# Kernel optimization log

Hardware: AMD Instinct MI355X
Metric: run time of the kernel (lower is better)

Reference implementation:

```python
import jax, jax.numpy as jnp
import numpy as np

TAU = 0.02
M = 5  # len(modality_types) + 1; modality 0 == padding


def setup_inputs() -> dict:
    B, Q, S, D = 64, 32, 256, 128
    key = jax.random.key(0)
    k0, k1, k2, k3, k4 = jax.random.split(key, 5)
    q = jax.random.normal(k0, (B, Q, D), dtype=jnp.float32)
    q = q / jnp.linalg.norm(q, axis=-1, keepdims=True)
    d = jax.random.normal(k1, (B, S, D), dtype=jnp.float32)
    d = d / jnp.linalg.norm(d, axis=-1, keepdims=True)
    # guarantee every modality 0..M-1 appears in each doc (first M tokens)
    head = jnp.tile(jnp.arange(M, dtype=jnp.int32), (B, 1))
    rest = jax.random.randint(k2, (B, S - M), 0, M, dtype=jnp.int32)
    modality_ids = jnp.concatenate([head, rest], axis=1)
    query_types = jax.random.randint(k3, (B,), 1, M, dtype=jnp.int32)  # in [1, M-1]
    lengths = jax.random.randint(k4, (B,), Q // 2, Q + 1)
    query_mask = jnp.arange(Q)[None, :] < lengths[:, None]
    return {"query_emb": q, "doc_emb": d, "modality_ids": modality_ids,
            "query_types": query_types, "query_mask": query_mask}


def _loss(query_emb, doc_emb, modality_ids, query_types, query_mask):
    B = query_emb.shape[0]
    idx = jnp.arange(B)
    # token-level similarity: (B, C, Q, S)
    base = jnp.einsum('bqd,csd->bcqs', query_emb, doc_emb)
    qnorm = jnp.maximum(query_mask.sum(axis=1), 1).astype(base.dtype)  # (B,)

    # agg (ColBERT max-sim): max over non-pad doc tokens, masked query sum
    nonpad = (modality_ids != 0)[None, :, None, :]
    agg_max = jnp.where(nonpad, base, -jnp.inf).max(axis=-1)           # (B, C, Q)
    sim = (agg_max * query_mask[:, None, :].astype(base.dtype)).sum(axis=-1)
    sim = sim / qnorm[:, None]                                          # (B, C)

    # _all_modality_sims: segmented max over s per modality, then sum over q
    per_mod = []
    for m in range(M):
        mask_m = (modality_ids == m)[None, :, None, :]
        per_mod.append(jnp.where(mask_m, base, -jnp.inf).max(axis=-1).sum(axis=-1))
    sims = jnp.stack(per_mod, axis=-1)                                  # (B, C, M)
    sims = sims / qnorm[:, None, None]

    # replace diagonal with the query's own modality score
    sim_fixed = sim.at[idx, idx].set(sims[idx, idx, query_types])

    # hard negatives: all (doc, modality) pairs except pad modality and own positive
    all_modal = sims.reshape(B, B * M)
    keep_mask = jnp.ones((B, B * M), dtype=bool)
    keep_mask = keep_mask.at[:, 0::M].set(False)
    keep_mask = keep_mask.at[idx, idx * M + query_types].set(False)
    n_keep = B * M - B - 1  # exact per-row count (query_types >= 1, no overlap)
    order = jnp.argsort((~keep_mask).astype(jnp.int32), axis=1, stable=True)[:, :n_keep]
    extras = jnp.take_along_axis(all_modal, order, axis=1)              # (B, n_keep)

    logits = jnp.concatenate([sim_fixed, extras], axis=1) / TAU
    # cross entropy with labels = arange(B) (positive is column b)
    return (jax.nn.logsumexp(logits, axis=1) - logits[idx, idx]).mean()


def reference(query_emb, doc_emb, modality_ids, query_types, query_mask):
    return _loss(query_emb, doc_emb, modality_ids, query_types, query_mask)
```

## Files before the change

kernel.cpp:

```cpp
#include <hip/hip_runtime.h>
#include <math.h>

#define TAU_F 0.02f
#define NB 64
#define NQ 32
#define NS 256
#define ND 128
#define MAXT 20
#define PERMSTRIDE 320

typedef __bf16 bf16x8 __attribute__((ext_vector_type(8)));
typedef float f32x4 __attribute__((ext_vector_type(4)));

#define OFF_TILEMOD 0u
#define OFF_TCOUNT  5120u
#define OFF_DFRAG   131072u
#define OFF_QFRAG   5373952u
#define OFF_SIMOUT  5898240u

__global__ __launch_bounds__(256) void
prep_frag_kernel(const float* __restrict__ qemb, const float* __restrict__ demb,
                 const int* __restrict__ mod,
                 __bf16* __restrict__ qfrag, __bf16* __restrict__ dfrag,
                 int* __restrict__ tilemod_g, int* __restrict__ tcount_g) {
    int blk = blockIdx.x;
    int tid = threadIdx.x;
    int lane = tid & 63, wv = tid >> 6;
    int quad = lane >> 4, li = lane & 15;

    if (blk >= NB) {
        int b = blk - NB;
#pragma unroll
        for (int i = 0; i < 2; ++i) {
            int combo = wv * 2 + i;
            int qt = combo >> 2, kc = combo & 3;
            int rowq = qt * 16 + li;
            int k0 = kc * 32 + quad * 8;
            const float* src = qemb + ((size_t)b * NQ + rowq) * ND + k0;
            float4 a = *(const float4*)src;
            float4 bq = *(const float4*)(src + 4);
            bf16x8 o;
            o[0] = (__bf16)a.x;  o[1] = (__bf16)a.y;  o[2] = (__bf16)a.z;  o[3] = (__bf16)a.w;
            o[4] = (__bf16)bq.x; o[5] = (__bf16)bq.y; o[6] = (__bf16)bq.z; o[7] = (__bf16)bq.w;
            *(bf16x8*)(qfrag + (((size_t)(b * 2 + qt) * 4 + kc) * 64 + lane) * 8) = o;
        }
        return;
    }

    int c = blk;
    __shared__ int smod[NS];
    __shared__ int sperm[PERMSTRIDE];
    __shared__ int counts[5], firsts[5], offs[5], padded[5];
    __shared__ int stilemod[MAXT];
    __shared__ int sT;

    if (tid < 5) { counts[tid] = 0; firsts[tid] = NS; }
    __syncthreads();
    int m_tok = mod[c * NS + tid];
    smod[tid] = m_tok;
    if (m_tok) { atomicAdd(&counts[m_tok], 1); atomicMin(&firsts[m_tok], tid); }
    __syncthreads();
    if (tid == 0) {
        int pos = 0;
        for (int m = 1; m <= 4; ++m) {
            offs[m] = pos;
            int p = (counts[m] + 15) & ~15;
            padded[m] = p;
            for (int t = pos >> 4; t < (pos + p) >> 4; ++t) stilemod[t] = m;
            pos += p;
        }
        sT = pos >> 4;
        tcount_g[c] = pos >> 4;
    }
    __syncthreads();
    if (m_tok) {
        int rank = 0;
        for (int s = 0; s < tid; ++s) rank += (smod[s] == m_tok);
        sperm[offs[m_tok] + rank] = tid;
    }
    if (tid < 4) {
        int m = tid + 1;
        for (int p = counts[m]; p < padded[m]; ++p) sperm[offs[m] + p] = firsts[m];
    }
    __syncthreads();
    int T = sT;
    if (tid < T) tilemod_g[c * MAXT + tid] = stilemod[tid];

    int kc = wv;
    int k0 = kc * 32 + quad * 8;
    for (int t = 0; t < T; ++t) {
        int srow = sperm[t * 16 + li];
        const float* src = demb + ((size_t)c * NS + srow) * ND + k0;
        float4 a = *(const float4*)src;
        float4 bq = *(const float4*)(src + 4);
        bf16x8 o;
        o[0] = (__bf16)a.x;  o[1] = (__bf16)a.y;  o[2] = (__bf16)a.z;  o[3] = (__bf16)a.w;
        o[4] = (__bf16)bq.x; o[5] = (__bf16)bq.y; o[6] = (__bf16)bq.z; o[7] = (__bf16)bq.w;
        *(bf16x8*)(dfrag + (((size_t)(c * MAXT + t) * 4 + kc) * 64 + lane) * 8) = o;
    }
}

__global__ __launch_bounds__(256) void
main_kernel(const __bf16* __restrict__ dfrag, const __bf16* __restrict__ qfrag,
            const int* __restrict__ tilemod, const int* __restrict__ tcount,
            const int* __restrict__ qmask, float* __restrict__ simout) {
    int blk = blockIdx.x;
    int c = blk >> 5;
    int bp = blk & 31;
    int b0 = bp * 2;
    int tid = threadIdx.x;
    int lane = tid & 63, wv = tid >> 6;

    bf16x8 bfrag[4][4];
#pragma unroll
    for (int qt = 0; qt < 4; ++qt) {
        int bg = b0 + (qt >> 1), qtl = qt & 1;
#pragma unroll
        for (int kc = 0; kc < 4; ++kc)
            bfrag[qt][kc] = *(const bf16x8*)(qfrag + (((size_t)(bg * 2 + qtl) * 4 + kc) * 64 + lane) * 8);
    }

    float vmax[4][4];
#pragma unroll
    for (int m = 0; m < 4; ++m)
#pragma unroll
        for (int qt = 0; qt < 4; ++qt) vmax[m][qt] = -1e30f;

    int T = tcount[c];
    for (int t = wv; t < T; t += 4) {
        bf16x8 af[4];
#pragma unroll
        for (int kc = 0; kc < 4; ++kc)
            af[kc] = *(const bf16x8*)(dfrag + (((size_t)(c * MAXT + t) * 4 + kc) * 64 + lane) * 8);
        float vv[4];
#pragma unroll
        for (int qt = 0; qt < 4; ++qt) {
            f32x4 acc = {0.f, 0.f, 0.f, 0.f};
#pragma unroll
            for (int kc = 0; kc < 4; ++kc)
                acc = __builtin_amdgcn_mfma_f32_16x16x32_bf16(af[kc], bfrag[qt][kc], acc, 0, 0, 0);
            float v = fmaxf(fmaxf(acc[0], acc[1]), fmaxf(acc[2], acc[3]));
            v = fmaxf(v, __shfl_xor(v, 16, 64));
            v = fmaxf(v, __shfl_xor(v, 32, 64));
            vv[qt] = v;
        }
        int tm = tilemod[c * MAXT + t];
        switch (tm) {
        case 1:
#pragma unroll
            for (int qt = 0; qt < 4; ++qt) vmax[0][qt] = fmaxf(vmax[0][qt], vv[qt]);
            break;
        case 2:
#pragma unroll
            for (int qt = 0; qt < 4; ++qt) vmax[1][qt] = fmaxf(vmax[1][qt], vv[qt]);
            break;
        case 3:
#pragma unroll
            for (int qt = 0; qt < 4; ++qt) vmax[2][qt] = fmaxf(vmax[2][qt], vv[qt]);
            break;
        default:
#pragma unroll
            for (int qt = 0; qt < 4; ++qt) vmax[3][qt] = fmaxf(vmax[3][qt], vv[qt]);
            break;
        }
    }

    __shared__ float lv[4][4][4][16];
    if (lane < 16) {
#pragma unroll
        for (int m = 0; m < 4; ++m)
#pragma unroll
            for (int qt = 0; qt < 4; ++qt) lv[wv][m][qt][lane] = vmax[m][qt];
    }
    __syncthreads();
    __shared__ float l2[4][4][16];
    {
        int m = tid >> 6, qt = (tid >> 4) & 3, qi = tid & 15;
        float v = fmaxf(fmaxf(lv[0][m][qt][qi], lv[1][m][qt][qi]),
                        fmaxf(lv[2][m][qt][qi], lv[3][m][qt][qi]));
        l2[m][qt][qi] = v;
    }
    __syncthreads();
    if (tid < 64) {
        int bl = tid >> 5, q = tid & 31;
        int qt = bl * 2 + (q >> 4), qi = q & 15;
        float m1 = l2[0][qt][qi], m2 = l2[1][qt][qi];
        float m3 = l2[2][qt][qi], m4 = l2[3][qt][qi];
        int b = b0 + bl;
        float agg = fmaxf(fmaxf(m1, m2), fmaxf(m3, m4));
        float s0 = (qmask[b * NQ + q] != 0) ? agg : 0.f;
        float s1 = m1, s2 = m2, s3 = m3, s4 = m4;
#pragma unroll
        for (int off = 16; off >= 1; off >>= 1) {
            s0 += __shfl_xor(s0, off, 64);
            s1 += __shfl_xor(s1, off, 64);
            s2 += __shfl_xor(s2, off, 64);
            s3 += __shfl_xor(s3, off, 64);
            s4 += __shfl_xor(s4, off, 64);
        }
        if (q == 0) {
            float* o = simout + ((size_t)b * NB + c) * 5;
            o[0] = s0; o[1] = s1; o[2] = s2; o[3] = s3; o[4] = s4;
        }
    }
}

__global__ void loss_kernel(const float* __restrict__ simout, const int* __restrict__ qtypes,
                            const int* __restrict__ qmask, float* __restrict__ out) {
    __shared__ float lloss[NB];
    int tid = threadIdx.x;
    int r = tid >> 2, i = tid & 3;
    int cnt = 0;
#pragma unroll
    for (int j = 0; j < 8; ++j) cnt += (qmask[r * NQ + i * 8 + j] != 0);
    cnt += __shfl_xor(cnt, 1, 64);
    cnt += __shfl_xor(cnt, 2, 64);
    float scale = 1.0f / (TAU_F * (float)(cnt > 0 ? cnt : 1));

    float mx = -1e30f;
    for (int cc = 0; cc < 16; ++cc) {
        int c = i * 16 + cc;
        const float* p = simout + ((size_t)r * NB + c) * 5;
#pragma unroll
        for (int j = 0; j < 5; ++j) {
            if (j == 0 && c == r) continue;
            mx = fmaxf(mx, p[j] * scale);
        }
    }
    mx = fmaxf(mx, __shfl_xor(mx, 1, 64));
    mx = fmaxf(mx, __shfl_xor(mx, 2, 64));
    float sum = 0.f;
    for (int cc = 0; cc < 16; ++cc) {
        int c = i * 16 + cc;
        const float* p = simout + ((size_t)r * NB + c) * 5;
#pragma unroll
        for (int j = 0; j < 5; ++j) {
            if (j == 0 && c == r) continue;
            sum += expf(p[j] * scale - mx);
        }
    }
    sum += __shfl_xor(sum, 1, 64);
    sum += __shfl_xor(sum, 2, 64);
    if (i == 0) {
        float pos = simout[((size_t)r * NB + r) * 5 + qtypes[r]] * scale;
        lloss[r] = logf(sum) + mx - pos;
    }
    __syncthreads();
    if (tid == 0) {
        float s = 0.f;
        for (int r2 = 0; r2 < NB; ++r2) s += lloss[r2];
        out[0] = s * (1.0f / NB);
    }
}

extern "C" void kernel_launch(void* const* d_in, const int* in_sizes, int n_in,
                              void* d_out, int out_size, void* d_ws, size_t ws_size,
                              hipStream_t stream) {
    const float* qemb   = (const float*)d_in[0];
    const float* demb   = (const float*)d_in[1];
    const int*   mod    = (const int*)d_in[2];
    const int*   qtypes = (const int*)d_in[3];
    const int*   qmask  = (const int*)d_in[4];

    char* ws = (char*)d_ws;
    int*    tilemod = (int*)(ws + OFF_TILEMOD);
    int*    tcount  = (int*)(ws + OFF_TCOUNT);
    __bf16* dfrag   = (__bf16*)(ws + OFF_DFRAG);
    __bf16* qfrag   = (__bf16*)(ws + OFF_QFRAG);
    float*  simout  = (float*)(ws + OFF_SIMOUT);

    prep_frag_kernel<<<2 * NB, 256, 0, stream>>>(qemb, demb, mod, qfrag, dfrag, tilemod, tcount);
    main_kernel<<<2048, 256, 0, stream>>>(dfrag, qfrag, tilemod, tcount, qmask, simout);
    loss_kernel<<<1, 256, 0, stream>>>(simout, qtypes, qmask, (float*)d_out);
}
```

Baseline: 103.2 us.

## Fuse loss into main kernel via last-block atomic counter; stage query fragments in LDS

The separate loss kernel is folded into the main kernel. A global atomic counter, reset in the prep kernel, picks the last block to finish, and that block computes the cross-entropy, removing one launch. Query fragments are now staged in shared memory instead of held in registers, MFMAs are reordered to loop over k-chunks outside query tiles, and launch bounds request 4 blocks per SM, all aiming to raise occupancy. The costs are extra LDS reads per MFMA, threadfence and atomic overhead, and a serial tail in the last block.

```diff
diff --git a/kernel.cpp b/kernel.cpp
--- a/kernel.cpp
+++ b/kernel.cpp
@@ -14,6 +14,7 @@
 
 #define OFF_TILEMOD 0u
 #define OFF_TCOUNT  5120u
+#define OFF_COUNTER 8192u
 #define OFF_DFRAG   131072u
 #define OFF_QFRAG   5373952u
 #define OFF_SIMOUT  5898240u
@@ -22,11 +23,14 @@
 prep_frag_kernel(const float* __restrict__ qemb, const float* __restrict__ demb,
                  const int* __restrict__ mod,
                  __bf16* __restrict__ qfrag, __bf16* __restrict__ dfrag,
-                 int* __restrict__ tilemod_g, int* __restrict__ tcount_g) {
+                 int* __restrict__ tilemod_g, int* __restrict__ tcount_g,
+                 int* __restrict__ counter) {
     int blk = blockIdx.x;
     int tid = threadIdx.x;
     int lane = tid & 63, wv = tid >> 6;
     int quad = lane >> 4, li = lane & 15;
+
+    if (blk == 0 && tid == 0) *counter = 0;
 
     if (blk >= NB) {
         int b = blk - NB;
@@ -100,10 +104,12 @@
     }
 }
 
-__global__ __launch_bounds__(256) void
+__global__ __launch_bounds__(256, 4) void
 main_kernel(const __bf16* __restrict__ dfrag, const __bf16* __restrict__ qfrag,
             const int* __restrict__ tilemod, const int* __restrict__ tcount,
-            const int* __restrict__ qmask, float* __restrict__ simout) {
+            const int* __restrict__ qmask, const int* __restrict__ qtypes,
+            float* __restrict__ simout, int* __restrict__ counter,
+            float* __restrict__ out) {
     int blk = blockIdx.x;
     int c = blk >> 5;
     int bp = blk & 31;
@@ -111,14 +117,16 @@
     int tid = threadIdx.x;
     int lane = tid & 63, wv = tid >> 6;
 
-    bf16x8 bfrag[4][4];
-#pragma unroll
-    for (int qt = 0; qt < 4; ++qt) {
+    __shared__ __bf16 sq[4][4][64 * 8];
+#pragma unroll
+    for (int j = 0; j < 4; ++j) {
+        int f = tid + 256 * j;
+        int qt = f >> 8, kc = (f >> 6) & 3, ln = f & 63;
         int bg = b0 + (qt >> 1), qtl = qt & 1;
-#pragma unroll
-        for (int kc = 0; kc < 4; ++kc)
-            bfrag[qt][kc] = *(const bf16x8*)(qfrag + (((size_t)(bg * 2 + qtl) * 4 + kc) * 64 + lane) * 8);
-    }
+        *(bf16x8*)&sq[qt][kc][ln * 8] =
+            *(const bf16x8*)(qfrag + (((size_t)(bg * 2 + qtl) * 4 + kc) * 64 + ln) * 8);
+    }
+    __syncthreads();
 
     float vmax[4][4];
 #pragma unroll
@@ -128,18 +136,20 @@
 
     int T = tcount[c];
     for (int t = wv; t < T; t += 4) {
-        bf16x8 af[4];
-#pragma unroll
-        for (int kc = 0; kc < 4; ++kc)
-            af[kc] = *(const bf16x8*)(dfrag + (((size_t)(c * MAXT + t) * 4 + kc) * 64 + lane) * 8);
+        f32x4 acc[4] = {{0.f,0.f,0.f,0.f},{0.f,0.f,0.f,0.f},{0.f,0.f,0.f,0.f},{0.f,0.f,0.f,0.f}};
+#pragma unroll
+        for (int kc = 0; kc < 4; ++kc) {
+            bf16x8 af = *(const bf16x8*)(dfrag + (((size_t)(c * MAXT + t) * 4 + kc) * 64 + lane) * 8);
+#pragma unroll
+            for (int qt = 0; qt < 4; ++qt) {
+                bf16x8 bq = *(const bf16x8*)&sq[qt][kc][lane * 8];
+                acc[qt] = __builtin_amdgcn_mfma_f32_16x16x32_bf16(af, bq, acc[qt], 0, 0, 0);
+            }
+        }
         float vv[4];
 #pragma unroll
         for (int qt = 0; qt < 4; ++qt) {
-            f32x4 acc = {0.f, 0.f, 0.f, 0.f};
-#pragma unroll
-            for (int kc = 0; kc < 4; ++kc)
-                acc = __builtin_amdgcn_mfma_f32_16x16x32_bf16(af[kc], bfrag[qt][kc], acc, 0, 0, 0);
-            float v = fmaxf(fmaxf(acc[0], acc[1]), fmaxf(acc[2], acc[3]));
+            float v = fmaxf(fmaxf(acc[qt][0], acc[qt][1]), fmaxf(acc[qt][2], acc[qt][3]));
             v = fmaxf(v, __shfl_xor(v, 16, 64));
             v = fmaxf(v, __shfl_xor(v, 32, 64));
             vv[qt] = v;
@@ -203,12 +213,18 @@
             o[0] = s0; o[1] = s1; o[2] = s2; o[3] = s3; o[4] = s4;
         }
     }
-}
-
-__global__ void loss_kernel(const float* __restrict__ simout, const int* __restrict__ qtypes,
-                            const int* __restrict__ qmask, float* __restrict__ out) {
+
+    __shared__ int isLast;
+    __threadfence();
+    if (tid == 0) {
+        int v = atomicAdd(counter, 1);
+        isLast = (v == (int)gridDim.x - 1);
+    }
+    __syncthreads();
+    if (!isLast) return;
+    __threadfence();
+
     __shared__ float lloss[NB];
-    int tid = threadIdx.x;
     int r = tid >> 2, i = tid & 3;
     int cnt = 0;
 #pragma unroll
@@ -219,11 +235,11 @@
 
     float mx = -1e30f;
     for (int cc = 0; cc < 16; ++cc) {
-        int c = i * 16 + cc;
-        const float* p = simout + ((size_t)r * NB + c) * 5;
+        int cx = i * 16 + cc;
+        const float* p = simout + ((size_t)r * NB + cx) * 5;
 #pragma unroll
         for (int j = 0; j < 5; ++j) {
-            if (j == 0 && c == r) continue;
+            if (j == 0 && cx == r) continue;
             mx = fmaxf(mx, p[j] * scale);
         }
     }
@@ -231,11 +247,11 @@
     mx = fmaxf(mx, __shfl_xor(mx, 2, 64));
     float sum = 0.f;
     for (int cc = 0; cc < 16; ++cc) {
-        int c = i * 16 + cc;
-        const float* p = simout + ((size_t)r * NB + c) * 5;
+        int cx = i * 16 + cc;
+        const float* p = simout + ((size_t)r * NB + cx) * 5;
 #pragma unroll
         for (int j = 0; j < 5; ++j) {
-            if (j == 0 && c == r) continue;
+            if (j == 0 && cx == r) continue;
             sum += expf(p[j] * scale - mx);
         }
     }
@@ -265,11 +281,13 @@
     char* ws = (char*)d_ws;
     int*    tilemod = (int*)(ws + OFF_TILEMOD);
     int*    tcount  = (int*)(ws + OFF_TCOUNT);
+    int*    counter = (int*)(ws + OFF_COUNTER);
     __bf16* dfrag   = (__bf16*)(ws + OFF_DFRAG);
     __bf16* qfrag   = (__bf16*)(ws + OFF_QFRAG);
     float*  simout  = (float*)(ws + OFF_SIMOUT);
 
-    prep_frag_kernel<<<2 * NB, 256, 0, stream>>>(qemb, demb, mod, qfrag, dfrag, tilemod, tcount);
-    main_kernel<<<2048, 256, 0, stream>>>(dfrag, qfrag, tilemod, tcount, qmask, simout);
-    loss_kernel<<<1, 256, 0, stream>>>(simout, qtypes, qmask, (float*)d_out);
+    prep_frag_kernel<<<2 * NB, 256, 0, stream>>>(qemb, demb, mod, qfrag, dfrag,
+                                                 tilemod, tcount, counter);
+    main_kernel<<<2048, 256, 0, stream>>>(dfrag, qfrag, tilemod, tcount, qmask,
+                                          qtypes, simout, counter, (float*)d_out);
 }
```

Result: slower. 230.4 us (+123.3%).

## Switch to 32x32x16 bf16 MFMA with 32-row modality tiles and remap block order

Applied to the files above, without the earlier changes.

Replaces 16x16x32 MFMA tiles with 32x32x16 ones. Doc tokens are padded per modality to multiples of 32, and the fragment layouts for queries and docs are reorganised to match. Each block now covers two queries with a single 32-row B fragment. Fewer tiles and reductions are needed, but padding waste grows because modalities round up to 32 tokens. Block-to-(c,b) mapping is also swizzled so concurrently running blocks touch different docs.

```diff
diff --git a/kernel.cpp b/kernel.cpp
--- a/kernel.cpp
+++ b/kernel.cpp
@@ -6,17 +6,17 @@
 #define NQ 32
 #define NS 256
 #define ND 128
-#define MAXT 20
-#define PERMSTRIDE 320
+#define MAXT 12
+#define PERMSTRIDE 384
 
 typedef __bf16 bf16x8 __attribute__((ext_vector_type(8)));
-typedef float f32x4 __attribute__((ext_vector_type(4)));
+typedef float f32x16 __attribute__((ext_vector_type(16)));
 
 #define OFF_TILEMOD 0u
-#define OFF_TCOUNT  5120u
-#define OFF_DFRAG   131072u
-#define OFF_QFRAG   5373952u
-#define OFF_SIMOUT  5898240u
+#define OFF_TCOUNT  4096u
+#define OFF_DFRAG   16384u
+#define OFF_QFRAG   6307840u
+#define OFF_SIMOUT  6832128u
 
 __global__ __launch_bounds__(256) void
 prep_frag_kernel(const float* __restrict__ qemb, const float* __restrict__ demb,
@@ -26,23 +26,21 @@
     int blk = blockIdx.x;
     int tid = threadIdx.x;
     int lane = tid & 63, wv = tid >> 6;
-    int quad = lane >> 4, li = lane & 15;
+    int li32 = lane & 31, kh = lane >> 5;
 
     if (blk >= NB) {
         int b = blk - NB;
 #pragma unroll
         for (int i = 0; i < 2; ++i) {
-            int combo = wv * 2 + i;
-            int qt = combo >> 2, kc = combo & 3;
-            int rowq = qt * 16 + li;
-            int k0 = kc * 32 + quad * 8;
-            const float* src = qemb + ((size_t)b * NQ + rowq) * ND + k0;
+            int kc = wv * 2 + i;
+            int k0 = kc * 16 + kh * 8;
+            const float* src = qemb + ((size_t)b * NQ + li32) * ND + k0;
             float4 a = *(const float4*)src;
             float4 bq = *(const float4*)(src + 4);
             bf16x8 o;
             o[0] = (__bf16)a.x;  o[1] = (__bf16)a.y;  o[2] = (__bf16)a.z;  o[3] = (__bf16)a.w;
             o[4] = (__bf16)bq.x; o[5] = (__bf16)bq.y; o[6] = (__bf16)bq.z; o[7] = (__bf16)bq.w;
-            *(bf16x8*)(qfrag + (((size_t)(b * 2 + qt) * 4 + kc) * 64 + lane) * 8) = o;
+            *(bf16x8*)(qfrag + (((size_t)b * 8 + kc) * 64 + lane) * 8) = o;
         }
         return;
     }
@@ -64,13 +62,13 @@
         int pos = 0;
         for (int m = 1; m <= 4; ++m) {
             offs[m] = pos;
-            int p = (counts[m] + 15) & ~15;
+            int p = (counts[m] + 31) & ~31;
             padded[m] = p;
-            for (int t = pos >> 4; t < (pos + p) >> 4; ++t) stilemod[t] = m;
+            for (int t = pos >> 5; t < (pos + p) >> 5; ++t) stilemod[t] = m;
             pos += p;
         }
-        sT = pos >> 4;
-        tcount_g[c] = pos >> 4;
+        sT = pos >> 5;
+        tcount_g[c] = pos >> 5;
     }
     __syncthreads();
     if (m_tok) {
@@ -86,17 +84,18 @@
     int T = sT;
     if (tid < T) tilemod_g[c * MAXT + tid] = stilemod[tid];
 
-    int kc = wv;
-    int k0 = kc * 32 + quad * 8;
-    for (int t = 0; t < T; ++t) {
-        int srow = sperm[t * 16 + li];
-        const float* src = demb + ((size_t)c * NS + srow) * ND + k0;
-        float4 a = *(const float4*)src;
-        float4 bq = *(const float4*)(src + 4);
-        bf16x8 o;
-        o[0] = (__bf16)a.x;  o[1] = (__bf16)a.y;  o[2] = (__bf16)a.z;  o[3] = (__bf16)a.w;
-        o[4] = (__bf16)bq.x; o[5] = (__bf16)bq.y; o[6] = (__bf16)bq.z; o[7] = (__bf16)bq.w;
-        *(bf16x8*)(dfrag + (((size_t)(c * MAXT + t) * 4 + kc) * 64 + lane) * 8) = o;
+    for (int kc = wv; kc < 8; kc += 4) {
+        int k0 = kc * 16 + kh * 8;
+        for (int t = 0; t < T; ++t) {
+            int srow = sperm[t * 32 + li32];
+            const float* src = demb + ((size_t)c * NS + srow) * ND + k0;
+            float4 a = *(const float4*)src;
+            float4 bq = *(const float4*)(src + 4);
+            bf16x8 o;
+            o[0] = (__bf16)a.x;  o[1] = (__bf16)a.y;  o[2] = (__bf16)a.z;  o[3] = (__bf16)a.w;
+            o[4] = (__bf16)bq.x; o[5] = (__bf16)bq.y; o[6] = (__bf16)bq.z; o[7] = (__bf16)bq.w;
+            *(bf16x8*)(dfrag + (((size_t)(c * MAXT + t) * 8 + kc) * 64 + lane) * 8) = o;
+        }
     }
 }
 
@@ -105,88 +104,72 @@
             const int* __restrict__ tilemod, const int* __restrict__ tcount,
             const int* __restrict__ qmask, float* __restrict__ simout) {
     int blk = blockIdx.x;
-    int c = blk >> 5;
-    int bp = blk & 31;
+    int c  = (blk & 7) * 8 + (blk >> 8);
+    int bp = (blk >> 3) & 31;
     int b0 = bp * 2;
     int tid = threadIdx.x;
     int lane = tid & 63, wv = tid >> 6;
 
-    bf16x8 bfrag[4][4];
-#pragma unroll
-    for (int qt = 0; qt < 4; ++qt) {
-        int bg = b0 + (qt >> 1), qtl = qt & 1;
-#pragma unroll
-        for (int kc = 0; kc < 4; ++kc)
-            bfrag[qt][kc] = *(const bf16x8*)(qfrag + (((size_t)(bg * 2 + qtl) * 4 + kc) * 64 + lane) * 8);
-    }
-
-    float vmax[4][4];
-#pragma unroll
-    for (int m = 0; m < 4; ++m)
-#pragma unroll
-        for (int qt = 0; qt < 4; ++qt) vmax[m][qt] = -1e30f;
+    bf16x8 bfrag[2][8];
+#pragma unroll
+    for (int bi = 0; bi < 2; ++bi)
+#pragma unroll
+        for (int kc = 0; kc < 8; ++kc)
+            bfrag[bi][kc] = *(const bf16x8*)(qfrag + (((size_t)(b0 + bi) * 8 + kc) * 64 + lane) * 8);
+
+    float vmax[2][4];
+#pragma unroll
+    for (int bi = 0; bi < 2; ++bi)
+#pragma unroll
+        for (int m = 0; m < 4; ++m) vmax[bi][m] = -1e30f;
 
     int T = tcount[c];
     for (int t = wv; t < T; t += 4) {
-        bf16x8 af[4];
-#pragma unroll
-        for (int kc = 0; kc < 4; ++kc)
-            af[kc] = *(const bf16x8*)(dfrag + (((size_t)(c * MAXT + t) * 4 + kc) * 64 + lane) * 8);
-        float vv[4];
-#pragma unroll
-        for (int qt = 0; qt < 4; ++qt) {
-            f32x4 acc = {0.f, 0.f, 0.f, 0.f};
-#pragma unroll
-            for (int kc = 0; kc < 4; ++kc)
-                acc = __builtin_amdgcn_mfma_f32_16x16x32_bf16(af[kc], bfrag[qt][kc], acc, 0, 0, 0);
-            float v = fmaxf(fmaxf(acc[0], acc[1]), fmaxf(acc[2], acc[3]));
-            v = fmaxf(v, __shfl_xor(v, 16, 64));
+        bf16x8 af[8];
+#pragma unroll
+        for (int kc = 0; kc < 8; ++kc)
+            af[kc] = *(const bf16x8*)(dfrag + (((size_t)(c * MAXT + t) * 8 + kc) * 64 + lane) * 8);
+        int tm = tilemod[c * MAXT + t];
+#pragma unroll
+        for (int bi = 0; bi < 2; ++bi) {
+            f32x16 acc = {0.f,0.f,0.f,0.f,0.f,0.f,0.f,0.f,0.f,0.f,0.f,0.f,0.f,0.f,0.f,0.f};
+#pragma unroll
+            for (int kc = 0; kc < 8; ++kc)
+                acc = __builtin_amdgcn_mfma_f32_32x32x16_bf16(af[kc], bfrag[bi][kc], acc, 0, 0, 0);
+            float v = acc[0];
+#pragma unroll
+            for (int r = 1; r < 16; ++r) v = fmaxf(v, acc[r]);
             v = fmaxf(v, __shfl_xor(v, 32, 64));
-            vv[qt] = v;
-        }
-        int tm = tilemod[c * MAXT + t];
-        switch (tm) {
-        case 1:
-#pragma unroll
-            for (int qt = 0; qt < 4; ++qt) vmax[0][qt] = fmaxf(vmax[0][qt], vv[qt]);
-            break;
-        case 2:
-#pragma unroll
-            for (int qt = 0; qt < 4; ++qt) vmax[1][qt] = fmaxf(vmax[1][qt], vv[qt]);
-            break;
-        case 3:
-#pragma unroll
-            for (int qt = 0; qt < 4; ++qt) vmax[2][qt] = fmaxf(vmax[2][qt], vv[qt]);
-            break;
-        default:
-#pragma unroll
-            for (int qt = 0; qt < 4; ++qt) vmax[3][qt] = fmaxf(vmax[3][qt], vv[qt]);
-            break;
-        }
-    }
-
-    __shared__ float lv[4][4][4][16];
-    if (lane < 16) {
-#pragma unroll
-        for (int m = 0; m < 4; ++m)
-#pragma unroll
-            for (int qt = 0; qt < 4; ++qt) lv[wv][m][qt][lane] = vmax[m][qt];
-    }
-    __syncthreads();
-    __shared__ float l2[4][4][16];
+            switch (tm) {
+            case 1:  vmax[bi][0] = fmaxf(vmax[bi][0], v); break;
+            case 2:  vmax[bi][1] = fmaxf(vmax[bi][1], v); break;
+            case 3:  vmax[bi][2] = fmaxf(vmax[bi][2], v); break;
+            default: vmax[bi][3] = fmaxf(vmax[bi][3], v); break;
+            }
+        }
+    }
+
+    __shared__ float lv[4][2][4][32];
+    if (lane < 32) {
+#pragma unroll
+        for (int bi = 0; bi < 2; ++bi)
+#pragma unroll
+            for (int m = 0; m < 4; ++m) lv[wv][bi][m][lane] = vmax[bi][m];
+    }
+    __syncthreads();
+    __shared__ float l2[2][4][32];
     {
-        int m = tid >> 6, qt = (tid >> 4) & 3, qi = tid & 15;
-        float v = fmaxf(fmaxf(lv[0][m][qt][qi], lv[1][m][qt][qi]),
-                        fmaxf(lv[2][m][qt][qi], lv[3][m][qt][qi]));
-        l2[m][qt][qi] = v;
+        int bi = tid >> 7, m = (tid >> 5) & 3, q = tid & 31;
+        float v = fmaxf(fmaxf(lv[0][bi][m][q], lv[1][bi][m][q]),
+                        fmaxf(lv[2][bi][m][q], lv[3][bi][m][q]));
+        l2[bi][m][q] = v;
     }
     __syncthreads();
     if (tid < 64) {
-        int bl = tid >> 5, q = tid & 31;
-        int qt = bl * 2 + (q >> 4), qi = q & 15;
-        float m1 = l2[0][qt][qi], m2 = l2[1][qt][qi];
-        float m3 = l2[2][qt][qi], m4 = l2[3][qt][qi];
-        int b = b0 + bl;
+        int bi = tid >> 5, q = tid & 31;
+        float m1 = l2[bi][0][q], m2 = l2[bi][1][q];
+        float m3 = l2[bi][2][q], m4 = l2[bi][3][q];
+        int b = b0 + bi;
         float agg = fmaxf(fmaxf(m1, m2), fmaxf(m3, m4));
         float s0 = (qmask[b * NQ + q] != 0) ? agg : 0.f;
         float s1 = m1, s2 = m2, s3 = m3, s4 = m4;
@@ -269,7 +252,8 @@
     __bf16* qfrag   = (__bf16*)(ws + OFF_QFRAG);
     float*  simout  = (float*)(ws + OFF_SIMOUT);
 
-    prep_frag_kernel<<<2 * NB, 256, 0, stream>>>(qemb, demb, mod, qfrag, dfrag, tilemod, tcount);
+    prep_frag_kernel<<<2 * NB, 256, 0, stream>>>(qemb, demb, mod, qfrag, dfrag,
+                                                 tilemod, tcount);
     main_kernel<<<2048, 256, 0, stream>>>(dfrag, qfrag, tilemod, tcount, qmask, simout);
     loss_kernel<<<1, 256, 0, stream>>>(simout, qtypes, qmask, (float*)d_out);
 }
```

After: 101.8 us. About the same (-1.3%).
